# Kernel tuning notes

Measured on AMD Instinct MI355X. Metric: run time of the kernel, lower is better.

The kernel has to match this reference:

```python
import jax, jax.numpy as jnp
import numpy as np

EPS = 1e-6


def _layernorm2d(x, w, b):
    # Normalize over channel dim (axis=1) per pixel; x: [B,C,H,W]
    mu = jnp.mean(x, axis=1, keepdims=True)
    var = jnp.var(x, axis=1, keepdims=True)
    xn = (x - mu) * jax.lax.rsqrt(var + EPS)
    return xn * w[None, :, None, None] + b[None, :, None, None]


def _conv1x1(x, w, b):
    # 1x1 conv == channel matmul; w: [Cout, Cin], x: [B,Cin,H,W]
    return jnp.einsum('oc,bchw->bohw', w, x) + b[None, :, None, None]


def setup_inputs() -> dict:
    key = jax.random.key(0)
    ks = jax.random.split(key, 8)
    B, C, H, W = 4, 64, 180, 320
    s = C ** -0.5  # keep projection weights at sane scale
    return {
        'x_l': jax.random.normal(ks[0], (B, C, H, W), jnp.float32),
        'x_r': jax.random.normal(ks[1], (B, C, H, W), jnp.float32),
        'ln_l_w': jnp.ones((C,), jnp.float32),
        'ln_l_b': jnp.zeros((C,), jnp.float32),
        'ln_r_w': jnp.ones((C,), jnp.float32),
        'ln_r_b': jnp.zeros((C,), jnp.float32),
        'wq_l': jax.random.normal(ks[2], (C, C), jnp.float32) * s,
        'bq_l': jnp.zeros((C,), jnp.float32),
        'wq_r': jax.random.normal(ks[3], (C, C), jnp.float32) * s,
        'bq_r': jnp.zeros((C,), jnp.float32),
        'wv_l': jax.random.normal(ks[4], (C, C), jnp.float32) * s,
        'bv_l': jnp.zeros((C,), jnp.float32),
        'wv_r': jax.random.normal(ks[5], (C, C), jnp.float32) * s,
        'bv_r': jnp.zeros((C,), jnp.float32),
        'beta': jax.random.normal(ks[6], (C,), jnp.float32) * 0.1,
        'gamma': jax.random.normal(ks[7], (C,), jnp.float32) * 0.1,
    }


def reference(x_l, x_r, ln_l_w, ln_l_b, ln_r_w, ln_r_b,
              wq_l, bq_l, wq_r, bq_r, wv_l, bv_l, wv_r, bv_r,
              beta, gamma):
    C = x_l.shape[1]
    scale = C ** -0.5
    # Q projections of LayerNorm'd inputs (Select stub == identity pass-through)
    Q_l = _conv1x1(_layernorm2d(x_l, ln_l_w, ln_l_b), wq_l, bq_l)  # [B,C,H,W]
    Q_r = _conv1x1(_layernorm2d(x_r, ln_r_w, ln_r_b), wq_r, bq_r)  # [B,C,H,W]
    V_l = _conv1x1(x_l, wv_l, bv_l)  # [B,C,H,W]
    V_r = _conv1x1(x_r, wv_r, bv_r)  # [B,C,H,W]
    # attention over width per row: [B,H,Wl,Wr]
    attn = jnp.einsum('bchw,bchv->bhwv', Q_l, Q_r) * scale
    # r -> l: softmax over Wr (last axis), contract with V_r
    F_r2l = jnp.einsum('bhwv,bchv->bchw', jax.nn.softmax(attn, axis=-1), V_r)
    # l -> r: softmax over Wl (axis=2 of attn), contract with V_l
    F_l2r = jnp.einsum('bhwv,bchw->bchv', jax.nn.softmax(attn, axis=2), V_l)
    out_l = x_l + F_r2l * beta[None, :, None, None]
    out_r = x_r + F_l2r * gamma[None, :, None, None]
    return (out_l, out_r)
```

## Files before the change

### kernel.cpp

```cpp
#include <hip/hip_runtime.h>


#define HWs  57600
#define CHWs 3686400
#define TOTs 14745600
#define RST  72
#define VST  328
#define PTS  36
#define NTH  768

typedef short bf16x8 __attribute__((ext_vector_type(8)));
typedef float f32x4  __attribute__((ext_vector_type(4)));
union FragU { uint4 q; unsigned short u[8]; bf16x8 v; };

__device__ __forceinline__ unsigned short f2bf(float f) {
  unsigned u = __float_as_uint(f);
  u += 0x7fffu + ((u >> 16) & 1u);
  return (unsigned short)(u >> 16);
}
__device__ __forceinline__ float bf2f(unsigned short s) {
  return __uint_as_float(((unsigned)s) << 16);
}
__device__ __forceinline__ unsigned fenc(float f) {
  unsigned u = __float_as_uint(f);
  return u ^ (0x80000000u | (unsigned)(-(int)(u >> 31)));
}
__device__ __forceinline__ float fdec(unsigned k) {
  return __uint_as_float(k ^ (0x80000000u | (unsigned)(-(int)((k >> 31) ^ 1u))));
}

__global__ __launch_bounds__(NTH, 2)
void sfam_kernel(
    const float* __restrict__ x_l, const float* __restrict__ x_r,
    const float* __restrict__ ln_l_w, const float* __restrict__ ln_l_b,
    const float* __restrict__ ln_r_w, const float* __restrict__ ln_r_b,
    const float* __restrict__ wq_l, const float* __restrict__ bq_l,
    const float* __restrict__ wq_r, const float* __restrict__ bq_r,
    const float* __restrict__ wv_l, const float* __restrict__ bv_l,
    const float* __restrict__ wv_r, const float* __restrict__ bv_r,
    const float* __restrict__ beta, const float* __restrict__ gamma,
    float* __restrict__ out)
{
  __shared__ __align__(16) unsigned short Rs[320*RST];
  __shared__ __align__(16) unsigned short Ks[320*RST];
  __shared__ __align__(16) unsigned short Vb[64*VST];
  __shared__ __align__(16) unsigned short Pt[12*16*PTS];
  __shared__ unsigned CMu[320];
  __shared__ float MU[640], RSd[640];
  __shared__ float c_arr[320];
  __shared__ float BB[128];

  const int bh = blockIdx.x;
  const int b = bh / 180, h = bh - b*180;
  const int base = b*CHWs + h*320;

  const int t = threadIdx.x;
  const int wave = t >> 6, lane = t & 63;
  const int p = lane & 15, g = lane >> 4;
  const int nwt = (wave < 8) ? 2 : 1;
  const int w0 = (wave < 8) ? wave*32 : 256 + (wave-8)*16;

  for (int w2 = t; w2 < 640; w2 += NTH) {
    const int side = (w2 >= 320);
    const int w = w2 - side*320;
    const float* xp = side ? x_r : x_l;
    unsigned short* dst = side ? Ks : Rs;
    float s0 = 0.f, q0 = 0.f, s1 = 0.f, q1 = 0.f;
    #pragma unroll
    for (int cb = 0; cb < 64; cb += 8) {
      FragU f;
      #pragma unroll
      for (int j = 0; j < 8; ++j) {
        const float v = xp[base + (cb+j)*HWs + w];
        if (cb < 32) { s0 += v; q0 += v*v; } else { s1 += v; q1 += v*v; }
        f.u[j] = f2bf(v);
      }
      *(uint4*)&dst[w*RST + cb] = f.q;
    }
    const float m  = (s0 + s1) * (1.f/64.f);
    const float vv = (q0 + q1) * (1.f/64.f) - m*m;
    MU[side*320 + w]  = m;
    RSd[side*320 + w] = rsqrtf(vv + 1e-6f);
  }
  if (t < 320) CMu[t] = 0u;
  if (t < 128) {
    const int o = t & 63;
    const float* wqp = (t < 64) ? wq_l : wq_r;
    const float* lwp = (t < 64) ? ln_l_w : ln_r_w;
    const float* lbp = (t < 64) ? ln_l_b : ln_r_b;
    const float* bqp = (t < 64) ? bq_l : bq_r;
    float s = bqp[o];
    for (int c = 0; c < 64; ++c) s += wqp[o*64+c]*lwp[c]*lbp[c];
    BB[t] = s;
  }
  __syncthreads();

  auto projV = [&](const float* wvp, const float* bvp, const unsigned short* src,
                   const float* mup, const float* rsp, bool inv) {
    bf16x8 bx[2][2];
    #pragma unroll
    for (int nt = 0; nt < 2; ++nt) if (nt < nwt) {
      const int w = w0 + nt*16 + p;
      const float mu = mup[w];
      const float sd = inv ? (1.0f / rsp[w]) : 0.f;
      #pragma unroll
      for (int kf = 0; kf < 2; ++kf) {
        FragU f; f.q = *(const uint4*)&src[w*RST + kf*32 + g*8];
        if (inv) {
          FragU rr;
          #pragma unroll
          for (int j = 0; j < 8; ++j) rr.u[j] = f2bf(bf2f(f.u[j])*sd + mu);
          bx[nt][kf] = rr.v;
        } else bx[nt][kf] = f.v;
      }
    }
    #pragma unroll
    for (int mt = 0; mt < 4; ++mt) {
      bf16x8 av2[2];
      #pragma unroll
      for (int kf = 0; kf < 2; ++kf) {
        FragU rr;
        #pragma unroll
        for (int j = 0; j < 8; ++j) rr.u[j] = f2bf(wvp[(mt*16+p)*64 + kf*32 + g*8 + j]);
        av2[kf] = rr.v;
      }
      f32x4 acc2[2];
      #pragma unroll
      for (int nt = 0; nt < 2; ++nt) acc2[nt] = (f32x4){0.f,0.f,0.f,0.f};
      #pragma unroll
      for (int nt = 0; nt < 2; ++nt) if (nt < nwt)
        #pragma unroll
        for (int kf = 0; kf < 2; ++kf)
          acc2[nt] = __builtin_amdgcn_mfma_f32_16x16x32_bf16(av2[kf], bx[nt][kf], acc2[nt], 0,0,0);
      #pragma unroll
      for (int nt = 0; nt < 2; ++nt) if (nt < nwt)
        #pragma unroll
        for (int r = 0; r < 4; ++r) {
          const int o = mt*16 + g*4 + r;
          Vb[o*VST + w0 + nt*16 + p] = f2bf(acc2[nt][r] + bvp[o]);
        }
    }
  };

  projV(wv_l, bv_l, Rs, MU, RSd, false);

  float cR[2][4];
  {
    bf16x8 qa[2][2];
    #pragma unroll
    for (int wt = 0; wt < 2; ++wt) if (wt < nwt) {
      const int w = w0 + wt*16 + p;
      const float mu = MU[w], rs = RSd[w];
      #pragma unroll
      for (int kf = 0; kf < 2; ++kf) {
        FragU f; f.q = *(const uint4*)&Rs[w*RST + kf*32 + g*8];
        FragU rr;
        #pragma unroll
        for (int j = 0; j < 8; ++j) rr.u[j] = f2bf((bf2f(f.u[j]) - mu) * rs);
        qa[wt][kf] = rr.v;
      }
    }
    f32x4 qacc[2][4];
    #pragma unroll
    for (int wt = 0; wt < 2; ++wt)
      #pragma unroll
      for (int ot = 0; ot < 4; ++ot) qacc[wt][ot] = (f32x4){0.f,0.f,0.f,0.f};
    #pragma unroll
    for (int ot = 0; ot < 4; ++ot) {
      bf16x8 bw2[2];
      #pragma unroll
      for (int kf = 0; kf < 2; ++kf) {
        FragU rr;
        #pragma unroll
        for (int j = 0; j < 8; ++j) {
          const int c = kf*32 + g*8 + j;
          rr.u[j] = f2bf(wq_l[(ot*16+p)*64 + c] * ln_l_w[c]);
        }
        bw2[kf] = rr.v;
      }
      #pragma unroll
      for (int wt = 0; wt < 2; ++wt) if (wt < nwt)
        #pragma unroll
        for (int kf = 0; kf < 2; ++kf)
          qacc[wt][ot] = __builtin_amdgcn_mfma_f32_16x16x32_bf16(qa[wt][kf], bw2[kf], qacc[wt][ot], 0,0,0);
    }
    #pragma unroll
    for (int wt = 0; wt < 2; ++wt) {
      #pragma unroll
      for (int r = 0; r < 4; ++r) cR[wt][r] = 0.f;
      if (wt < nwt) {
        #pragma unroll
        for (int ot = 0; ot < 4; ++ot) {
          const float bl = BB[ot*16+p], br = BB[64 + ot*16+p];
          #pragma unroll
          for (int r = 0; r < 4; ++r) {
            const float qv = qacc[wt][ot][r] + bl;
            Rs[(w0 + wt*16 + g*4 + r)*RST + ot*16 + p] = f2bf(qv);
            cR[wt][r] += qv * br;
          }
        }
        #pragma unroll
        for (int r = 0; r < 4; ++r) {
          float cv = cR[wt][r];
          cv += __shfl_xor(cv, 1); cv += __shfl_xor(cv, 2);
          cv += __shfl_xor(cv, 4); cv += __shfl_xor(cv, 8);
          cv *= 0.125f;
          cR[wt][r] = cv;
          if (p == 0) c_arr[w0 + wt*16 + g*4 + r] = cv;
        }
      }
    }
  }

  {
    bf16x8 qla[2][2];
    #pragma unroll
    for (int wt = 0; wt < 2; ++wt) if (wt < nwt)
      #pragma unroll
      for (int kf = 0; kf < 2; ++kf) {
        FragU f; f.q = *(const uint4*)&Rs[(w0 + wt*16 + p)*RST + kf*32 + g*8];
        qla[wt][kf] = f.v;
      }
    f32x4 q2[2][4];
    #pragma unroll
    for (int wt = 0; wt < 2; ++wt)
      #pragma unroll
      for (int ct = 0; ct < 4; ++ct) q2[wt][ct] = (f32x4){0.f,0.f,0.f,0.f};
    #pragma unroll
    for (int ct = 0; ct < 4; ++ct) {
      const float lw = ln_r_w[ct*16 + p];
      bf16x8 bwt2[2];
      #pragma unroll
      for (int kf = 0; kf < 2; ++kf) {
        FragU rr;
        #pragma unroll
        for (int j = 0; j < 8; ++j)
          rr.u[j] = f2bf(wq_r[(kf*32 + g*8 + j)*64 + ct*16 + p] * lw);
        bwt2[kf] = rr.v;
      }
      #pragma unroll
      for (int wt = 0; wt < 2; ++wt) if (wt < nwt)
        #pragma unroll
        for (int kf = 0; kf < 2; ++kf)
          q2[wt][ct] = __builtin_amdgcn_mfma_f32_16x16x32_bf16(qla[wt][kf], bwt2[kf], q2[wt][ct], 0,0,0);
    }
    #pragma unroll
    for (int wt = 0; wt < 2; ++wt) if (wt < nwt)
      #pragma unroll
      for (int ct = 0; ct < 4; ++ct)
        #pragma unroll
        for (int r = 0; r < 4; ++r)
          Rs[(w0 + wt*16 + g*4 + r)*RST + ct*16 + p] = f2bf(q2[wt][ct][r] * 0.125f);
  }

  #pragma unroll
  for (int wt = 0; wt < 2; ++wt) if (wt < nwt) {
    const int w = w0 + wt*16 + p;
    const float mu = MU[320+w], rs = RSd[320+w];
    #pragma unroll
    for (int kf = 0; kf < 2; ++kf) {
      FragU f; f.q = *(const uint4*)&Ks[w*RST + kf*32 + g*8];
      FragU rr;
      #pragma unroll
      for (int j = 0; j < 8; ++j) rr.u[j] = f2bf((bf2f(f.u[j]) - mu) * rs);
      *(uint4*)&Ks[w*RST + kf*32 + g*8] = rr.q;
    }
  }
  __syncthreads();

  bf16x8 aq[2][2];
  #pragma unroll
  for (int wt = 0; wt < 2; ++wt) if (wt < nwt)
    #pragma unroll
    for (int kf = 0; kf < 2; ++kf) {
      FragU f1; f1.q = *(const uint4*)&Rs[(w0 + wt*16 + p)*RST + kf*32 + g*8];
      aq[wt][kf] = f1.v;
    }

  float rmx[2][4];
  #pragma unroll
  for (int wt = 0; wt < 2; ++wt)
    #pragma unroll
    for (int r = 0; r < 4; ++r) rmx[wt][r] = -3.0e38f;
  for (int ch = 0; ch < 5; ++ch) {
    const int k0 = ch*64;
    #pragma unroll
    for (int vt = 0; vt < 4; ++vt) {
      FragU f0, f1;
      f0.q = *(const uint4*)&Ks[(k0 + vt*16 + p)*RST + g*8];
      f1.q = *(const uint4*)&Ks[(k0 + vt*16 + p)*RST + 32 + g*8];
      f32x4 s0 = (f32x4){0.f,0.f,0.f,0.f};
      s0 = __builtin_amdgcn_mfma_f32_16x16x32_bf16(aq[0][0], f0.v, s0, 0,0,0);
      s0 = __builtin_amdgcn_mfma_f32_16x16x32_bf16(aq[0][1], f1.v, s0, 0,0,0);
      float cp = -3.0e38f;
      #pragma unroll
      for (int r = 0; r < 4; ++r) {
        const float v0 = s0[r] + cR[0][r];
        rmx[0][r] = fmaxf(rmx[0][r], v0);
        cp = fmaxf(cp, v0);
      }
      if (nwt > 1) {
        f32x4 s1 = (f32x4){0.f,0.f,0.f,0.f};
        s1 = __builtin_amdgcn_mfma_f32_16x16x32_bf16(aq[1][0], f0.v, s1, 0,0,0);
        s1 = __builtin_amdgcn_mfma_f32_16x16x32_bf16(aq[1][1], f1.v, s1, 0,0,0);
        #pragma unroll
        for (int r = 0; r < 4; ++r) {
          const float v1 = s1[r] + cR[1][r];
          rmx[1][r] = fmaxf(rmx[1][r], v1);
          cp = fmaxf(cp, v1);
        }
      }
      cp = fmaxf(cp, __shfl_xor(cp, 16));
      cp = fmaxf(cp, __shfl_xor(cp, 32));
      if (g == 0) atomicMax(&CMu[k0 + vt*16 + p], fenc(cp));
    }
  }
  float rm[2][4];
  #pragma unroll
  for (int wt = 0; wt < 2; ++wt)
    #pragma unroll
    for (int r = 0; r < 4; ++r) {
      float m = rmx[wt][r];
      m = fmaxf(m, __shfl_xor(m, 1)); m = fmaxf(m, __shfl_xor(m, 2));
      m = fmaxf(m, __shfl_xor(m, 4)); m = fmaxf(m, __shfl_xor(m, 8));
      rm[wt][r] = m;
    }
  __syncthreads();

  float ls[2][4];
  f32x4 oacc[2][4];
  auto attn_pass = [&](bf16x8 (&A)[2][2], const unsigned short* Bsrc,
                       float (&mx)[2][4], bool colc) {
    float rsa[2][4];
    #pragma unroll
    for (int wt = 0; wt < 2; ++wt)
      #pragma unroll
      for (int r = 0; r < 4; ++r) rsa[wt][r] = 0.f;
    unsigned short* ptw = &Pt[wave*16*PTS];
    for (int ch = 0; ch < 5; ++ch) {
      const int k0 = ch*64;
      #pragma unroll
      for (int pvk = 0; pvk < 2; ++pvk) {
        bf16x8 bq2[2][2];
        #pragma unroll
        for (int vh = 0; vh < 2; ++vh)
          #pragma unroll
          for (int kf = 0; kf < 2; ++kf) {
            FragU f; f.q = *(const uint4*)&Bsrc[(k0 + (pvk*2+vh)*16 + p)*RST + kf*32 + g*8];
            bq2[vh][kf] = f.v;
          }
        float cc2[2];
        #pragma unroll
        for (int vh = 0; vh < 2; ++vh)
          cc2[vh] = colc ? c_arr[k0 + (pvk*2+vh)*16 + p] : 0.f;
        f32x4 sa[2][2];
        #pragma unroll
        for (int wt = 0; wt < 2; ++wt)
          #pragma unroll
          for (int vh = 0; vh < 2; ++vh) sa[wt][vh] = (f32x4){0.f,0.f,0.f,0.f};
        #pragma unroll
        for (int wt = 0; wt < 2; ++wt) if (wt < nwt)
          #pragma unroll
          for (int vh = 0; vh < 2; ++vh)
            #pragma unroll
            for (int kf = 0; kf < 2; ++kf)
              sa[wt][vh] = __builtin_amdgcn_mfma_f32_16x16x32_bf16(A[wt][kf], bq2[vh][kf], sa[wt][vh], 0,0,0);
        #pragma unroll
        for (int wt = 0; wt < 2; ++wt) if (wt < nwt) {
          #pragma unroll
          for (int r = 0; r < 4; ++r) {
            const float rc = colc ? 0.f : cR[wt][r];
            #pragma unroll
            for (int vh = 0; vh < 2; ++vh) {
              const float e = __expf(sa[wt][vh][r] + rc + cc2[vh] - mx[wt][r]);
              sa[wt][vh][r] = e;
              rsa[wt][r] += e;
            }
          }
        }
        bf16x8 bvv[4];
        #pragma unroll
        for (int ot = 0; ot < 4; ++ot) {
          FragU f; f.q = *(const uint4*)&Vb[(ot*16+p)*VST + k0 + pvk*32 + g*8];
          bvv[ot] = f.v;
        }
        #pragma unroll
        for (int wt = 0; wt < 2; ++wt) if (wt < nwt) {
          #pragma unroll
          for (int vh = 0; vh < 2; ++vh)
            #pragma unroll
            for (int r = 0; r < 4; ++r)
              ptw[(g*4 + r)*PTS + vh*16 + p] = f2bf(sa[wt][vh][r]);
          FragU fa; fa.q = *(const uint4*)&ptw[p*PTS + g*8];
          #pragma unroll
          for (int ot = 0; ot < 4; ++ot)
            oacc[wt][ot] = __builtin_amdgcn_mfma_f32_16x16x32_bf16(fa.v, bvv[ot], oacc[wt][ot], 0,0,0);
        }
      }
    }
    #pragma unroll
    for (int wt = 0; wt < 2; ++wt)
      #pragma unroll
      for (int r = 0; r < 4; ++r) {
        float s = rsa[wt][r];
        s += __shfl_xor(s, 1); s += __shfl_xor(s, 2);
        s += __shfl_xor(s, 4); s += __shfl_xor(s, 8);
        ls[wt][r] = s;
      }
  };

  bf16x8 ak[2][2];
  #pragma unroll
  for (int wt = 0; wt < 2; ++wt) if (wt < nwt)
    #pragma unroll
    for (int kf = 0; kf < 2; ++kf) {
      FragU f2; f2.q = *(const uint4*)&Ks[(w0 + wt*16 + p)*RST + kf*32 + g*8];
      ak[wt][kf] = f2.v;
    }
  float cmR[2][4];
  #pragma unroll
  for (int wt = 0; wt < 2; ++wt)
    #pragma unroll
    for (int r = 0; r < 4; ++r)
      cmR[wt][r] = (wt < nwt) ? fdec(CMu[w0 + wt*16 + g*4 + r]) : 0.f;
  #pragma unroll
  for (int wt = 0; wt < 2; ++wt)
    #pragma unroll
    for (int ot = 0; ot < 4; ++ot) oacc[wt][ot] = (f32x4){0.f,0.f,0.f,0.f};
  attn_pass(ak, Rs, cmR, true);
  __syncthreads();

  #pragma unroll
  for (int wt = 0; wt < 2; ++wt) if (wt < nwt)
    #pragma unroll
    for (int r = 0; r < 4; ++r) {
      const float inv = 1.0f / ls[wt][r];
      #pragma unroll
      for (int ot = 0; ot < 4; ++ot)
        Rs[(w0 + wt*16 + g*4 + r)*RST + ot*16 + p] = f2bf(oacc[wt][ot][r] * inv);
    }

  projV(wv_r, bv_r, Ks, MU+320, RSd+320, true);
  __syncthreads();

  #pragma unroll
  for (int wt = 0; wt < 2; ++wt)
    #pragma unroll
    for (int ot = 0; ot < 4; ++ot) oacc[wt][ot] = (f32x4){0.f,0.f,0.f,0.f};
  attn_pass(aq, Ks, rm, false);
  __syncthreads();

  #pragma unroll
  for (int wt = 0; wt < 2; ++wt) if (wt < nwt)
    #pragma unroll
    for (int r = 0; r < 4; ++r) {
      const float inv = 1.0f / ls[wt][r];
      #pragma unroll
      for (int ot = 0; ot < 4; ++ot)
        Ks[(w0 + wt*16 + g*4 + r)*RST + ot*16 + p] = f2bf(oacc[wt][ot][r] * inv);
    }
  __syncthreads();

  for (int w2 = t; w2 < 640; w2 += NTH) {
    const int side = (w2 >= 320);
    const int w = w2 - side*320;
    const float* xs = side ? x_r : x_l;
    const unsigned short* Osrc = side ? Rs : Ks;
    const float* sc = side ? gamma : beta;
    float* op = out + (side ? TOTs : 0);
    #pragma unroll
    for (int cb = 0; cb < 64; cb += 8) {
      FragU f; f.q = *(const uint4*)&Osrc[w*RST + cb];
      #pragma unroll
      for (int j = 0; j < 8; ++j) {
        const int cc = cb + j;
        const int gi = base + cc*HWs + w;
        op[gi] = xs[gi] + sc[cc] * bf2f(f.u[j]);
      }
    }
  }
}

extern "C" void kernel_launch(void* const* d_in, const int* in_sizes, int n_in,
                              void* d_out, int out_size, void* d_ws, size_t ws_size,
                              hipStream_t stream) {
  (void)in_sizes; (void)n_in; (void)d_ws; (void)ws_size; (void)out_size;
  sfam_kernel<<<dim3(720), dim3(NTH), 0, stream>>>(
      (const float*)d_in[0],  (const float*)d_in[1],
      (const float*)d_in[2],  (const float*)d_in[3],
      (const float*)d_in[4],  (const float*)d_in[5],
      (const float*)d_in[6],  (const float*)d_in[7],
      (const float*)d_in[8],  (const float*)d_in[9],
      (const float*)d_in[10], (const float*)d_in[11],
      (const float*)d_in[12], (const float*)d_in[13],
      (const float*)d_in[14], (const float*)d_in[15],
      (float*)d_out);
}
```

Baseline: 426.5 us.

## Replace exact softmax max pre-pass with Cauchy-Schwarz upper bounds

Removes the separate QK^T pass that computed exact row and column maxima for both softmaxes. It uses upper bounds instead: the norm of each Q row times the largest normalized-K norm for the row max, and a per-column norm plus the global max Q norm and bias term for the column max. Per-block maxima are gathered with shared-memory atomics. This drops a full score MFMA sweep and a barrier, but a loose bound could make the exponentials underflow and lose accuracy. Dropping the row bias term cR from the exponent is valid because a per-row constant cancels in the row softmax.

```diff
diff --git a/kernel.cpp b/kernel.cpp
--- a/kernel.cpp
+++ b/kernel.cpp
@@ -45,10 +45,11 @@
   __shared__ __align__(16) unsigned short Ks[320*RST];
   __shared__ __align__(16) unsigned short Vb[64*VST];
   __shared__ __align__(16) unsigned short Pt[12*16*PTS];
-  __shared__ unsigned CMu[320];
+  __shared__ float NX[320];
   __shared__ float MU[640], RSd[640];
   __shared__ float c_arr[320];
   __shared__ float BB[128];
+  __shared__ unsigned SCu[3];
 
   const int bh = blockIdx.x;
   const int b = bh / 180, h = bh - b*180;
@@ -59,6 +60,8 @@
   const int p = lane & 15, g = lane >> 4;
   const int nwt = (wave < 8) ? 2 : 1;
   const int w0 = (wave < 8) ? wave*32 : 256 + (wave-8)*16;
+
+  if (t < 3) SCu[t] = 0u;
 
   for (int w2 = t; w2 < 640; w2 += NTH) {
     const int side = (w2 >= 320);
@@ -81,8 +84,13 @@
     const float vv = (q0 + q1) * (1.f/64.f) - m*m;
     MU[side*320 + w]  = m;
     RSd[side*320 + w] = rsqrtf(vv + 1e-6f);
-  }
-  if (t < 320) CMu[t] = 0u;
+    if (side) {
+      const float vc = fmaxf(vv, 0.f);
+      const float nx = 8.f * sqrtf(vc / (vc + 1e-6f));
+      NX[w] = nx;
+      atomicMax(&SCu[0], fenc(nx));
+    }
+  }
   if (t < 128) {
     const int o = t & 63;
     const float* wqp = (t < 64) ? wq_l : wq_r;
@@ -206,12 +214,16 @@
           cv += __shfl_xor(cv, 4); cv += __shfl_xor(cv, 8);
           cv *= 0.125f;
           cR[wt][r] = cv;
-          if (p == 0) c_arr[w0 + wt*16 + g*4 + r] = cv;
-        }
-      }
-    }
-  }
-
+          if (p == 0) {
+            c_arr[w0 + wt*16 + g*4 + r] = cv;
+            atomicMax(&SCu[2], fenc(cv));
+          }
+        }
+      }
+    }
+  }
+
+  float rm[2][4];
   {
     bf16x8 qla[2][2];
     #pragma unroll
@@ -244,13 +256,28 @@
         for (int kf = 0; kf < 2; ++kf)
           q2[wt][ct] = __builtin_amdgcn_mfma_f32_16x16x32_bf16(qla[wt][kf], bwt2[kf], q2[wt][ct], 0,0,0);
     }
-    #pragma unroll
-    for (int wt = 0; wt < 2; ++wt) if (wt < nwt)
-      #pragma unroll
-      for (int ct = 0; ct < 4; ++ct)
-        #pragma unroll
-        for (int r = 0; r < 4; ++r)
-          Rs[(w0 + wt*16 + g*4 + r)*RST + ct*16 + p] = f2bf(q2[wt][ct][r] * 0.125f);
+    const float NXmax = fdec(SCu[0]);
+    #pragma unroll
+    for (int wt = 0; wt < 2; ++wt) {
+      #pragma unroll
+      for (int r = 0; r < 4; ++r) rm[wt][r] = 0.f;
+      if (wt < nwt) {
+        #pragma unroll
+        for (int r = 0; r < 4; ++r) {
+          float qsq = 0.f;
+          #pragma unroll
+          for (int ct = 0; ct < 4; ++ct) {
+            const float qv = q2[wt][ct][r] * 0.125f;
+            Rs[(w0 + wt*16 + g*4 + r)*RST + ct*16 + p] = f2bf(qv);
+            qsq += qv*qv;
+          }
+          qsq += __shfl_xor(qsq, 1); qsq += __shfl_xor(qsq, 2);
+          qsq += __shfl_xor(qsq, 4); qsq += __shfl_xor(qsq, 8);
+          rm[wt][r] = sqrtf(qsq) * NXmax;
+          if (p == 0) atomicMax(&SCu[1], fenc(qsq));
+        }
+      }
+    }
   }
 
   #pragma unroll
@@ -276,56 +303,6 @@
       FragU f1; f1.q = *(const uint4*)&Rs[(w0 + wt*16 + p)*RST + kf*32 + g*8];
       aq[wt][kf] = f1.v;
     }
-
-  float rmx[2][4];
-  #pragma unroll
-  for (int wt = 0; wt < 2; ++wt)
-    #pragma unroll
-    for (int r = 0; r < 4; ++r) rmx[wt][r] = -3.0e38f;
-  for (int ch = 0; ch < 5; ++ch) {
-    const int k0 = ch*64;
-    #pragma unroll
-    for (int vt = 0; vt < 4; ++vt) {
-      FragU f0, f1;
-      f0.q = *(const uint4*)&Ks[(k0 + vt*16 + p)*RST + g*8];
-      f1.q = *(const uint4*)&Ks[(k0 + vt*16 + p)*RST + 32 + g*8];
-      f32x4 s0 = (f32x4){0.f,0.f,0.f,0.f};
-      s0 = __builtin_amdgcn_mfma_f32_16x16x32_bf16(aq[0][0], f0.v, s0, 0,0,0);
-      s0 = __builtin_amdgcn_mfma_f32_16x16x32_bf16(aq[0][1], f1.v, s0, 0,0,0);
-      float cp = -3.0e38f;
-      #pragma unroll
-      for (int r = 0; r < 4; ++r) {
-        const float v0 = s0[r] + cR[0][r];
-        rmx[0][r] = fmaxf(rmx[0][r], v0);
-        cp = fmaxf(cp, v0);
-      }
-      if (nwt > 1) {
-        f32x4 s1 = (f32x4){0.f,0.f,0.f,0.f};
-        s1 = __builtin_amdgcn_mfma_f32_16x16x32_bf16(aq[1][0], f0.v, s1, 0,0,0);
-        s1 = __builtin_amdgcn_mfma_f32_16x16x32_bf16(aq[1][1], f1.v, s1, 0,0,0);
-        #pragma unroll
-        for (int r = 0; r < 4; ++r) {
-          const float v1 = s1[r] + cR[1][r];
-          rmx[1][r] = fmaxf(rmx[1][r], v1);
-          cp = fmaxf(cp, v1);
-        }
-      }
-      cp = fmaxf(cp, __shfl_xor(cp, 16));
-      cp = fmaxf(cp, __shfl_xor(cp, 32));
-      if (g == 0) atomicMax(&CMu[k0 + vt*16 + p], fenc(cp));
-    }
-  }
-  float rm[2][4];
-  #pragma unroll
-  for (int wt = 0; wt < 2; ++wt)
-    #pragma unroll
-    for (int r = 0; r < 4; ++r) {
-      float m = rmx[wt][r];
-      m = fmaxf(m, __shfl_xor(m, 1)); m = fmaxf(m, __shfl_xor(m, 2));
-      m = fmaxf(m, __shfl_xor(m, 4)); m = fmaxf(m, __shfl_xor(m, 8));
-      rm[wt][r] = m;
-    }
-  __syncthreads();
 
   float ls[2][4];
   f32x4 oacc[2][4];
@@ -369,10 +346,9 @@
         for (int wt = 0; wt < 2; ++wt) if (wt < nwt) {
           #pragma unroll
           for (int r = 0; r < 4; ++r) {
-            const float rc = colc ? 0.f : cR[wt][r];
             #pragma unroll
             for (int vh = 0; vh < 2; ++vh) {
-              const float e = __expf(sa[wt][vh][r] + rc + cc2[vh] - mx[wt][r]);
+              const float e = __expf(sa[wt][vh][r] + cc2[vh] - mx[wt][r]);
               sa[wt][vh][r] = e;
               rsa[wt][r] += e;
             }
@@ -418,11 +394,15 @@
       ak[wt][kf] = f2.v;
     }
   float cmR[2][4];
-  #pragma unroll
-  for (int wt = 0; wt < 2; ++wt)
-    #pragma unroll
-    for (int r = 0; r < 4; ++r)
-      cmR[wt][r] = (wt < nwt) ? fdec(CMu[w0 + wt*16 + g*4 + r]) : 0.f;
+  {
+    const float Qnmax = sqrtf(fdec(SCu[1]));
+    const float Cmax  = fdec(SCu[2]);
+    #pragma unroll
+    for (int wt = 0; wt < 2; ++wt)
+      #pragma unroll
+      for (int r = 0; r < 4; ++r)
+        cmR[wt][r] = (wt < nwt) ? NX[w0 + wt*16 + g*4 + r] * Qnmax + Cmax : 0.f;
+  }
   #pragma unroll
   for (int wt = 0; wt < 2; ++wt)
     #pragma unroll
```

Result: faster. 416.1 us (-2.4%).
